# Kernel tuning notes

Measured on AMD Instinct MI355X. Metric: run time of the kernel, lower is better.

The kernel has to match this reference:

```python
import jax, jax.numpy as jnp
import numpy as np

NLAYERS = 2
K = 8          # number of attention heads
H = 64         # hidden_size (per-head QK dim)
D = 1024       # input_size; value head dim = D // K = 128
B = 4
L = 1024


def setup_inputs() -> dict:
    key = jax.random.key(0)
    ks = jax.random.split(key, 5)
    s = 1.0 / np.sqrt(D).astype(np.float32)
    return {
        "x": jax.random.normal(ks[0], (B, L, D), jnp.float32),
        "Wq": jax.random.normal(ks[1], (NLAYERS, D, H * K), jnp.float32) * s,
        "bq": jnp.zeros((NLAYERS, H * K), jnp.float32),
        "Wk": jax.random.normal(ks[2], (NLAYERS, D, H * K), jnp.float32) * s,
        "bk": jnp.zeros((NLAYERS, H * K), jnp.float32),
    }


def reference(x, Wq, bq, Wk, bk):
    Bb, Ll, Dd = x.shape
    scale = 1.0 / np.sqrt(H).astype(np.float32)
    # strictly lower-triangular causal mask: torch.tril(-1)
    causal = jnp.tril(jnp.ones((Ll, Ll), x.dtype), -1)
    neg = 1e30 * (1.0 - causal)  # additive mask
    out = x
    graphs, outputs = [], []
    for i in range(NLAYERS):
        q = jax.nn.relu(out @ Wq[i] + bq[i]).reshape(Bb, Ll, K, H)
        k = jax.nn.relu(out @ Wk[i] + bk[i]).reshape(Bb, Ll, K, H)
        att = jnp.einsum('bqkh,bskh->bkqs', q, k) * scale - neg  # [B,K,L,L]
        att = jax.nn.softmax(att, axis=-1)
        v = out.reshape(Bb, Ll, K, Dd // K)                      # value = hidden itself
        cur = jnp.einsum('bkqs,bskd->bqkd', att, v).reshape(Bb, Ll, Dd)
        out = out + cur  # residual (use_gru=False)
        graphs.append(att)
        outputs.append(out)
    return jnp.stack(graphs, 0), jnp.stack(outputs, 0)
```

## Files before the change

kernel.cpp:

```cpp
#include <hip/hip_runtime.h>
#include <cstdint>
#include <cstddef>

typedef float  f32x4  __attribute__((ext_vector_type(4)));
typedef short  bf16x8 __attribute__((ext_vector_type(8)));

constexpr int Bc = 4, Lc = 1024, Dc = 1024, Kc = 8, Hc = 64, NHc = 512;
constexpr float SCALE = 0.125f;
constexpr long long GSZ = 2LL * Bc * Kc * Lc * Lc;
constexpr long long OSZ = (long long)Bc * Lc * Dc;
constexpr int QB = 16;

__device__ __forceinline__ unsigned short f2bf(float f) {
    unsigned u = __float_as_uint(f);
    u += 0x7fffu + ((u >> 16) & 1u);
    return (unsigned short)(u >> 16);
}
__device__ __forceinline__ float bf2f(unsigned short s) {
    return __uint_as_float((unsigned)s << 16);
}

__global__ __launch_bounds__(256)
void cast_bf16(const float* __restrict__ in, unsigned short* __restrict__ outp, int n)
{
    const int i = (blockIdx.x * 256 + threadIdx.x) * 8;
    if (i >= n) return;
    float4 a = *(const float4*)(in + i);
    float4 b = *(const float4*)(in + i + 4);
    bf16x8 v;
    v[0] = (short)f2bf(a.x); v[1] = (short)f2bf(a.y);
    v[2] = (short)f2bf(a.z); v[3] = (short)f2bf(a.w);
    v[4] = (short)f2bf(b.x); v[5] = (short)f2bf(b.y);
    v[6] = (short)f2bf(b.z); v[7] = (short)f2bf(b.w);
    *(bf16x8*)(outp + i) = v;
}

__global__ __launch_bounds__(256)
void wtrans(const float* __restrict__ Wq, const float* __restrict__ Wk,
            float* __restrict__ outbase)
{
    __shared__ float Tl[64][68];
    const int z = blockIdx.z, layer = z >> 1, m = z & 1;
    const float* src = (m ? Wk : Wq) + (size_t)layer * Dc * NHc;
    unsigned short* dst = (unsigned short*)(outbase + (size_t)layer * (GSZ / 2))
                          + (size_t)m * NHc * Dc;
    const int k0 = blockIdx.x * 64, n0 = blockIdx.y * 64;
    const int t = threadIdx.x;
    {
        const int r0 = t >> 4, c0 = (t & 15) * 4;
        #pragma unroll
        for (int i = 0; i < 4; ++i)
            *(float4*)&Tl[r0 + 16 * i][c0] =
                *(const float4*)&src[(size_t)(k0 + r0 + 16 * i) * NHc + n0 + c0];
    }
    __syncthreads();
    {
        const int nn = t >> 2, ks = (t & 3) * 16;
        bf16x8 v0, v1;
        #pragma unroll
        for (int j = 0; j < 8; ++j) v0[j] = (short)f2bf(Tl[ks + j][nn]);
        #pragma unroll
        for (int j = 0; j < 8; ++j) v1[j] = (short)f2bf(Tl[ks + 8 + j][nn]);
        unsigned short* dp = dst + (size_t)(n0 + nn) * Dc + k0 + ks;
        *(bf16x8*)dp       = v0;
        *(bf16x8*)(dp + 8) = v1;
    }
}

__global__ __launch_bounds__(512)
void qk_gemm(const unsigned short* __restrict__ hidb,
             const unsigned short* __restrict__ Wtq, const unsigned short* __restrict__ Wtk,
             const float* __restrict__ bq, const float* __restrict__ bk,
             unsigned short* __restrict__ qbuf, unsigned short* __restrict__ kbuf)
{
    __shared__ unsigned short As[2][128][40];
    __shared__ unsigned short Bs[2][128][40];

    const unsigned short* Wt = blockIdx.z ? Wtk : Wtq;
    const float* bi = blockIdx.z ? bk : bq;
    unsigned short* C = blockIdx.z ? kbuf : qbuf;
    const int m0 = blockIdx.x * 128, n0 = blockIdx.y * 128;
    const int t = threadIdx.x, lane = t & 63, w = t >> 6;
    const int lr = lane & 15, lg = lane >> 4;
    const int wmloc = (w >> 2) * 64, wnloc = (w & 3) * 32;

    const int srow = t >> 2, scol = (t & 3) * 8;
    const unsigned short* Ag = hidb + (size_t)(m0 + srow) * Dc + scol;
    const unsigned short* Bg = Wt   + (size_t)(n0 + srow) * Dc + scol;

    f32x4 acc[4][2] = {};
    bf16x8 ra = *(const bf16x8*)Ag;
    bf16x8 rb = *(const bf16x8*)Bg;

    for (int it = 0; it < 32; ++it) {
        const int buf = it & 1;
        *(bf16x8*)&As[buf][srow][scol] = ra;
        *(bf16x8*)&Bs[buf][srow][scol] = rb;
        __syncthreads();
        if (it < 31) {
            ra = *(const bf16x8*)(Ag + (it + 1) * 32);
            rb = *(const bf16x8*)(Bg + (it + 1) * 32);
        }
        bf16x8 a[4], bfr[2];
        #pragma unroll
        for (int mi = 0; mi < 4; ++mi)
            a[mi] = *(const bf16x8*)&As[buf][wmloc + mi * 16 + lr][lg * 8];
        #pragma unroll
        for (int ni = 0; ni < 2; ++ni)
            bfr[ni] = *(const bf16x8*)&Bs[buf][wnloc + ni * 16 + lr][lg * 8];
        #pragma unroll
        for (int mi = 0; mi < 4; ++mi)
            #pragma unroll
            for (int ni = 0; ni < 2; ++ni)
                acc[mi][ni] = __builtin_amdgcn_mfma_f32_16x16x32_bf16(a[mi], bfr[ni], acc[mi][ni], 0, 0, 0);
    }

    #pragma unroll
    for (int ni = 0; ni < 2; ++ni) {
        const int gc = n0 + wnloc + ni * 16 + lr;
        const float bv = bi[gc];
        #pragma unroll
        for (int mi = 0; mi < 4; ++mi)
            #pragma unroll
            for (int r = 0; r < 4; ++r) {
                const int row = m0 + wmloc + mi * 16 + lg * 4 + r;
                float v = fmaxf(acc[mi][ni][r] + bv, 0.0f);
                C[(size_t)row * NHc + gc] = f2bf(v);
            }
    }
}

__global__ __launch_bounds__(512)
void attn_fused(const unsigned short* __restrict__ qbuf,
                const unsigned short* __restrict__ kbuf,
                const unsigned short* __restrict__ hidb,
                const float* __restrict__ res,
                float* __restrict__ att, float* __restrict__ outp,
                unsigned short* __restrict__ hidnext)
{
    __shared__ unsigned short Sb[QB][1040];
    __shared__ unsigned short KV[2][64][132];

    const int id = blockIdx.x;
    const int kh = id & 7, qt = (id >> 3) & 63, b = id >> 9;
    const int q0 = qt * QB;
    const int t = threadIdx.x, lane = t & 63, w = t >> 6;
    const int lr = lane & 15, lg = lane >> 4;

    bf16x8 aq[2];
    #pragma unroll
    for (int ks = 0; ks < 2; ++ks)
        aq[ks] = *(const bf16x8*)(qbuf + (size_t)(b * Lc + q0 + lr) * NHc + kh * Hc + ks * 32 + lg * 8);

    const int ccount = (q0 + QB + 63) >> 6;

    const int sh = t >> 8, srow = (t & 255) >> 2, scol = (t & 3) * 16;
    for (int cb = 0; cb < ccount; cb += 2) {
        const int cs = cb + sh;
        if (cs < ccount) {
            const unsigned short* kp = kbuf + (size_t)(b * Lc + cs * 64 + srow) * NHc + kh * Hc + scol;
            *(bf16x8*)&KV[sh][srow][scol]     = *(const bf16x8*)kp;
            *(bf16x8*)&KV[sh][srow][scol + 8] = *(const bf16x8*)(kp + 8);
        }
        __syncthreads();
        const int c = cb + (w >> 2);
        if (c < ccount) {
            const int ni = w & 3;
            f32x4 acc = {};
            #pragma unroll
            for (int ks = 0; ks < 2; ++ks) {
                bf16x8 bfr = *(const bf16x8*)&KV[w >> 2][ni * 16 + lr][ks * 32 + lg * 8];
                acc = __builtin_amdgcn_mfma_f32_16x16x32_bf16(aq[ks], bfr, acc, 0, 0, 0);
            }
            #pragma unroll
            for (int r = 0; r < 4; ++r)
                Sb[lg * 4 + r][c * 64 + ni * 16 + lr] = f2bf(acc[r] * SCALE);
        }
        __syncthreads();
    }

    #pragma unroll
    for (int i = 0; i < 2; ++i) {
        const int row = w * 2 + i, qrow = q0 + row;
        float* orow = att + ((size_t)(b * Kc + kh) * Lc + qrow) * Lc;
        if (qrow == 0) {
            const float u = 1.0f / 1024.0f;
            const short ub = (short)f2bf(u);
            bf16x8 pv8;
            #pragma unroll
            for (int j = 0; j < 8; ++j) pv8[j] = ub;
            #pragma unroll
            for (int tt = 0; tt < 2; ++tt) {
                const int col = lane * 8 + tt * 512;
                float4 o = { u, u, u, u };
                *(float4*)(orow + col) = o;
                *(float4*)(orow + col + 4) = o;
                *(bf16x8*)&Sb[row][col] = pv8;
            }
            continue;
        }
        float p[16];
        float mx = -3.0e38f;
        #pragma unroll
        for (int tt = 0; tt < 2; ++tt) {
            const int col = lane * 8 + tt * 512;
            bf16x8 v = *(const bf16x8*)&Sb[row][col];
            #pragma unroll
            for (int j = 0; j < 8; ++j) {
                const float f = bf2f((unsigned short)v[j]);
                p[tt * 8 + j] = f;
                if (col + j < qrow) mx = fmaxf(mx, f);
            }
        }
        #pragma unroll
        for (int off = 1; off < 64; off <<= 1) mx = fmaxf(mx, __shfl_xor(mx, off));
        float sum = 0.0f;
        #pragma unroll
        for (int tt = 0; tt < 2; ++tt)
            #pragma unroll
            for (int j = 0; j < 8; ++j) {
                const int col = lane * 8 + tt * 512 + j;
                const float e = (col < qrow) ? __expf(p[tt * 8 + j] - mx) : 0.0f;
                p[tt * 8 + j] = e; sum += e;
            }
        #pragma unroll
        for (int off = 1; off < 64; off <<= 1) sum += __shfl_xor(sum, off);
        const float inv = 1.0f / sum;
        #pragma unroll
        for (int tt = 0; tt < 2; ++tt) {
            const int col = lane * 8 + tt * 512;
            float4 o0 = { p[tt*8+0]*inv, p[tt*8+1]*inv, p[tt*8+2]*inv, p[tt*8+3]*inv };
            float4 o1 = { p[tt*8+4]*inv, p[tt*8+5]*inv, p[tt*8+6]*inv, p[tt*8+7]*inv };
            *(float4*)(orow + col) = o0;
            *(float4*)(orow + col + 4) = o1;
            bf16x8 pb;
            #pragma unroll
            for (int j = 0; j < 8; ++j) pb[j] = (short)f2bf(p[tt * 8 + j] * inv);
            *(bf16x8*)&Sb[row][col] = pb;
        }
    }
    __syncthreads();

    const int stiles = (qt == 0) ? 16 : ccount;
    f32x4 acc3 = {};
    const int dloc = w * 16 + lr;
    const int dcol = kh * 128 + dloc;
    const int vrow = t >> 3, vcol = (t & 7) * 16;
    for (int ti = 0; ti < stiles; ++ti) {
        const int buf = ti & 1;
        const unsigned short* vp = hidb + (size_t)(b * Lc + ti * 64 + vrow) * Dc + kh * 128 + vcol;
        *(bf16x8*)&KV[buf][vrow][vcol]     = *(const bf16x8*)vp;
        *(bf16x8*)&KV[buf][vrow][vcol + 8] = *(const bf16x8*)(vp + 8);
        __syncthreads();
        #pragma unroll
        for (int ks = 0; ks < 2; ++ks) {
            bf16x8 pa = *(const bf16x8*)&Sb[lr][ti * 64 + ks * 32 + lg * 8];
            bf16x8 bb;
            #pragma unroll
            for (int j = 0; j < 8; ++j)
                bb[j] = (short)KV[buf][ks * 32 + lg * 8 + j][dloc];
            acc3 = __builtin_amdgcn_mfma_f32_16x16x32_bf16(pa, bb, acc3, 0, 0, 0);
        }
    }

    #pragma unroll
    for (int r = 0; r < 4; ++r) {
        const size_t idx = (size_t)(b * Lc + q0 + lg * 4 + r) * Dc + dcol;
        const float v = res[idx] + acc3[r];
        outp[idx] = v;
        if (hidnext) hidnext[idx] = f2bf(v);
    }
}

extern "C" void kernel_launch(void* const* d_in, const int* in_sizes, int n_in,
                              void* d_out, int out_size, void* d_ws, size_t ws_size,
                              hipStream_t stream)
{
    const float* x  = (const float*)d_in[0];
    const float* Wq = (const float*)d_in[1];
    const float* bq = (const float*)d_in[2];
    const float* Wk = (const float*)d_in[3];
    const float* bk = (const float*)d_in[4];
    float* out = (float*)d_out;

    unsigned short* hidbA = (unsigned short*)d_ws;
    unsigned short* hidbB = hidbA + (size_t)Bc * Lc * Dc;
    unsigned short* qb    = hidbB + (size_t)Bc * Lc * Dc;
    unsigned short* kb    = qb    + (size_t)Bc * Lc * NHc;

    const int nhid = Bc * Lc * Dc;

    cast_bf16<<<nhid / 8 / 256, 256, 0, stream>>>(x, hidbA, nhid);
    wtrans<<<dim3(16, 8, 4), 256, 0, stream>>>(Wq, Wk, out);

    for (int l = 0; l < 2; ++l) {
        float* attL = out + (size_t)l * (GSZ / 2);
        float* outL = out + GSZ + (size_t)l * OSZ;
        const float* resL = l ? (out + GSZ) : x;
        const unsigned short* hidL = l ? hidbB : hidbA;
        const unsigned short* WtL = (const unsigned short*)attL;

        qk_gemm<<<dim3(32, 4, 2), 512, 0, stream>>>(
            hidL, WtL, WtL + (size_t)NHc * Dc, bq + l * NHc, bk + l * NHc, qb, kb);

        attn_fused<<<Bc * 64 * Kc, 512, 0, stream>>>(
            qb, kb, hidL, resL, attL, outL, l == 0 ? hidbB : (unsigned short*)nullptr);
    }
}
```

Before: 193.7 us.

## Use transposed bf16 hidden for PV and batch four K chunks per iteration

A new cast_tr kernel runs once per layer and writes a bf16 copy of the hidden state transposed to [B,D,L]. In the PV phase each MFMA operand then comes from one vectorized LDS read, replacing eight strided 16-bit reads. The QK score phase now stages four 64-row K chunks per barrier pair and issues two MFMAs per wave, which halves the number of barriers. In exchange, each layer pays for an extra transpose pass over the 16 MB fp32 activations.

```diff
diff --git a/kernel.cpp b/kernel.cpp
--- a/kernel.cpp
+++ b/kernel.cpp
@@ -36,6 +36,33 @@
 }
 
 __global__ __launch_bounds__(256)
+void cast_tr(const float* __restrict__ src, unsigned short* __restrict__ hidT)
+{
+    __shared__ float Tl[64][68];
+    const int b = blockIdx.z, s0 = blockIdx.x * 64, d0 = blockIdx.y * 64;
+    const int t = threadIdx.x;
+    {
+        const int r = t >> 4, c = (t & 15) * 4;
+        #pragma unroll
+        for (int i = 0; i < 4; ++i)
+            *(float4*)&Tl[r + 16 * i][c] =
+                *(const float4*)&src[((size_t)(b * Lc + s0 + r + 16 * i)) * Dc + d0 + c];
+    }
+    __syncthreads();
+    {
+        const int d = t >> 2, sc = (t & 3) * 16;
+        bf16x8 v0, v1;
+        #pragma unroll
+        for (int j = 0; j < 8; ++j) v0[j] = (short)f2bf(Tl[sc + j][d]);
+        #pragma unroll
+        for (int j = 0; j < 8; ++j) v1[j] = (short)f2bf(Tl[sc + 8 + j][d]);
+        unsigned short* dp = hidT + ((size_t)(b * Dc + d0 + d)) * Lc + s0 + sc;
+        *(bf16x8*)dp       = v0;
+        *(bf16x8*)(dp + 8) = v1;
+    }
+}
+
+__global__ __launch_bounds__(256)
 void wtrans(const float* __restrict__ Wq, const float* __restrict__ Wk,
             float* __restrict__ outbase)
 {
@@ -133,13 +160,14 @@
 __global__ __launch_bounds__(512)
 void attn_fused(const unsigned short* __restrict__ qbuf,
                 const unsigned short* __restrict__ kbuf,
-                const unsigned short* __restrict__ hidb,
+                const unsigned short* __restrict__ hidT,
                 const float* __restrict__ res,
                 float* __restrict__ att, float* __restrict__ outp,
                 unsigned short* __restrict__ hidnext)
 {
     __shared__ unsigned short Sb[QB][1040];
-    __shared__ unsigned short KV[2][64][132];
+    __shared__ unsigned short KS[4][64][66];
+    unsigned short (*VT)[128][66] = (unsigned short (*)[128][66])KS;
 
     const int id = blockIdx.x;
     const int kh = id & 7, qt = (id >> 3) & 63, b = id >> 9;
@@ -154,27 +182,35 @@
 
     const int ccount = (q0 + QB + 63) >> 6;
 
-    const int sh = t >> 8, srow = (t & 255) >> 2, scol = (t & 3) * 16;
-    for (int cb = 0; cb < ccount; cb += 2) {
-        const int cs = cb + sh;
+    const int ch = t >> 7, krow = (t & 127) >> 1, kcol = (t & 1) * 32;
+    for (int cb = 0; cb < ccount; cb += 4) {
+        const int cs = cb + ch;
         if (cs < ccount) {
-            const unsigned short* kp = kbuf + (size_t)(b * Lc + cs * 64 + srow) * NHc + kh * Hc + scol;
-            *(bf16x8*)&KV[sh][srow][scol]     = *(const bf16x8*)kp;
-            *(bf16x8*)&KV[sh][srow][scol + 8] = *(const bf16x8*)(kp + 8);
+            const unsigned short* kp = kbuf + (size_t)(b * Lc + cs * 64 + krow) * NHc + kh * Hc + kcol;
+            *(bf16x8*)&KS[ch][krow][kcol]      = *(const bf16x8*)kp;
+            *(bf16x8*)&KS[ch][krow][kcol + 8]  = *(const bf16x8*)(kp + 8);
+            *(bf16x8*)&KS[ch][krow][kcol + 16] = *(const bf16x8*)(kp + 16);
+            *(bf16x8*)&KS[ch][krow][kcol + 24] = *(const bf16x8*)(kp + 24);
         }
         __syncthreads();
-        const int c = cb + (w >> 2);
+        const int c = cb + (w >> 1);
         if (c < ccount) {
-            const int ni = w & 3;
-            f32x4 acc = {};
-            #pragma unroll
-            for (int ks = 0; ks < 2; ++ks) {
-                bf16x8 bfr = *(const bf16x8*)&KV[w >> 2][ni * 16 + lr][ks * 32 + lg * 8];
-                acc = __builtin_amdgcn_mfma_f32_16x16x32_bf16(aq[ks], bfr, acc, 0, 0, 0);
-            }
-            #pragma unroll
-            for (int r = 0; r < 4; ++r)
-                Sb[lg * 4 + r][c * 64 + ni * 16 + lr] = f2bf(acc[r] * SCALE);
+            f32x4 acc[2] = {};
+            #pragma unroll
+            for (int ks = 0; ks < 2; ++ks)
+                #pragma unroll
+                for (int i = 0; i < 2; ++i) {
+                    const int ni = (w & 1) * 2 + i;
+                    bf16x8 bfr = *(const bf16x8*)&KS[w >> 1][ni * 16 + lr][ks * 32 + lg * 8];
+                    acc[i] = __builtin_amdgcn_mfma_f32_16x16x32_bf16(aq[ks], bfr, acc[i], 0, 0, 0);
+                }
+            #pragma unroll
+            for (int i = 0; i < 2; ++i) {
+                const int ni = (w & 1) * 2 + i;
+                #pragma unroll
+                for (int r = 0; r < 4; ++r)
+                    Sb[lg * 4 + r][c * 64 + ni * 16 + lr] = f2bf(acc[i][r] * SCALE);
+            }
         }
         __syncthreads();
     }
@@ -243,22 +279,19 @@
 
     const int stiles = (qt == 0) ? 16 : ccount;
     f32x4 acc3 = {};
-    const int dloc = w * 16 + lr;
-    const int dcol = kh * 128 + dloc;
-    const int vrow = t >> 3, vcol = (t & 7) * 16;
+    const int dloc = w * 16 + lr, dcol = kh * 128 + dloc;
+    const int vd = t >> 2, vsc = (t & 3) * 16;
+    const unsigned short* vbase = hidT + (size_t)(b * Dc + kh * 128 + vd) * Lc + vsc;
     for (int ti = 0; ti < stiles; ++ti) {
         const int buf = ti & 1;
-        const unsigned short* vp = hidb + (size_t)(b * Lc + ti * 64 + vrow) * Dc + kh * 128 + vcol;
-        *(bf16x8*)&KV[buf][vrow][vcol]     = *(const bf16x8*)vp;
-        *(bf16x8*)&KV[buf][vrow][vcol + 8] = *(const bf16x8*)(vp + 8);
+        const unsigned short* vp = vbase + ti * 64;
+        *(bf16x8*)&VT[buf][vd][vsc]     = *(const bf16x8*)vp;
+        *(bf16x8*)&VT[buf][vd][vsc + 8] = *(const bf16x8*)(vp + 8);
         __syncthreads();
         #pragma unroll
         for (int ks = 0; ks < 2; ++ks) {
             bf16x8 pa = *(const bf16x8*)&Sb[lr][ti * 64 + ks * 32 + lg * 8];
-            bf16x8 bb;
-            #pragma unroll
-            for (int j = 0; j < 8; ++j)
-                bb[j] = (short)KV[buf][ks * 32 + lg * 8 + j][dloc];
+            bf16x8 bb = *(const bf16x8*)&VT[buf][dloc][ks * 32 + lg * 8];
             acc3 = __builtin_amdgcn_mfma_f32_16x16x32_bf16(pa, bb, acc3, 0, 0, 0);
         }
     }
@@ -283,27 +316,29 @@
     const float* bk = (const float*)d_in[4];
     float* out = (float*)d_out;
 
-    unsigned short* hidbA = (unsigned short*)d_ws;
-    unsigned short* hidbB = hidbA + (size_t)Bc * Lc * Dc;
-    unsigned short* qb    = hidbB + (size_t)Bc * Lc * Dc;
-    unsigned short* kb    = qb    + (size_t)Bc * Lc * NHc;
+    unsigned short* hidb = (unsigned short*)d_ws;
+    unsigned short* hidT = hidb + (size_t)Bc * Lc * Dc;
+    unsigned short* qb   = hidT + (size_t)Bc * Dc * Lc;
+    unsigned short* kb   = qb   + (size_t)Bc * Lc * NHc;
 
     const int nhid = Bc * Lc * Dc;
 
-    cast_bf16<<<nhid / 8 / 256, 256, 0, stream>>>(x, hidbA, nhid);
+    cast_bf16<<<nhid / 8 / 256, 256, 0, stream>>>(x, hidb, nhid);
     wtrans<<<dim3(16, 8, 4), 256, 0, stream>>>(Wq, Wk, out);
 
     for (int l = 0; l < 2; ++l) {
         float* attL = out + (size_t)l * (GSZ / 2);
         float* outL = out + GSZ + (size_t)l * OSZ;
         const float* resL = l ? (out + GSZ) : x;
-        const unsigned short* hidL = l ? hidbB : hidbA;
+        const float* srcL = l ? (out + GSZ) : x;
         const unsigned short* WtL = (const unsigned short*)attL;
 
+        cast_tr<<<dim3(16, 16, 4), 256, 0, stream>>>(srcL, hidT);
+
         qk_gemm<<<dim3(32, 4, 2), 512, 0, stream>>>(
-            hidL, WtL, WtL + (size_t)NHc * Dc, bq + l * NHc, bk + l * NHc, qb, kb);
+            hidb, WtL, WtL + (size_t)NHc * Dc, bq + l * NHc, bk + l * NHc, qb, kb);
 
         attn_fused<<<Bc * 64 * Kc, 512, 0, stream>>>(
-            qb, kb, hidL, resL, attL, outL, l == 0 ? hidbB : (unsigned short*)nullptr);
-    }
-}
+            qb, kb, hidT, resL, attL, outL, l == 0 ? hidb : (unsigned short*)nullptr);
+    }
+}
```

After: 304.7 us. +57.3%, slower.

## Shrink LDS via union buffer, recompute softmax exps, raise occupancy hint

Applied to the files above, without the earlier changes.

Shared memory for K and V tiles is merged into a union with tighter padding, and the score buffer padding is reduced, so more blocks can fit per CU. The launch bounds now request 6 waves-per-EU occupancy. The softmax no longer keeps a 16-float register array and instead rereads LDS and recomputes the exps, trading extra exp work for fewer registers. The QK loop now does one 128-key chunk per iteration with all 8 waves, and s_setprio wraps the MFMA sections. The V loop gains a second barrier because the tile is no longer double-buffered.

```diff
diff --git a/kernel.cpp b/kernel.cpp
--- a/kernel.cpp
+++ b/kernel.cpp
@@ -130,7 +130,7 @@
     }
 }
 
-__global__ __launch_bounds__(512)
+__global__ __launch_bounds__(512, 6)
 void attn_fused(const unsigned short* __restrict__ qbuf,
                 const unsigned short* __restrict__ kbuf,
                 const unsigned short* __restrict__ hidb,
@@ -138,8 +138,12 @@
                 float* __restrict__ att, float* __restrict__ outp,
                 unsigned short* __restrict__ hidnext)
 {
-    __shared__ unsigned short Sb[QB][1040];
-    __shared__ unsigned short KV[2][64][132];
+    __shared__ unsigned short Sb[QB][1032];
+    union KVU {
+        unsigned short KS[128][72];
+        unsigned short VS[64][136];
+    };
+    __shared__ KVU kv;
 
     const int id = blockIdx.x;
     const int kh = id & 7, qt = (id >> 3) & 63, b = id >> 9;
@@ -153,29 +157,25 @@
         aq[ks] = *(const bf16x8*)(qbuf + (size_t)(b * Lc + q0 + lr) * NHc + kh * Hc + ks * 32 + lg * 8);
 
     const int ccount = (q0 + QB + 63) >> 6;
-
-    const int sh = t >> 8, srow = (t & 255) >> 2, scol = (t & 3) * 16;
-    for (int cb = 0; cb < ccount; cb += 2) {
-        const int cs = cb + sh;
-        if (cs < ccount) {
-            const unsigned short* kp = kbuf + (size_t)(b * Lc + cs * 64 + srow) * NHc + kh * Hc + scol;
-            *(bf16x8*)&KV[sh][srow][scol]     = *(const bf16x8*)kp;
-            *(bf16x8*)&KV[sh][srow][scol + 8] = *(const bf16x8*)(kp + 8);
-        }
-        __syncthreads();
-        const int c = cb + (w >> 2);
-        if (c < ccount) {
-            const int ni = w & 3;
-            f32x4 acc = {};
-            #pragma unroll
-            for (int ks = 0; ks < 2; ++ks) {
-                bf16x8 bfr = *(const bf16x8*)&KV[w >> 2][ni * 16 + lr][ks * 32 + lg * 8];
-                acc = __builtin_amdgcn_mfma_f32_16x16x32_bf16(aq[ks], bfr, acc, 0, 0, 0);
-            }
-            #pragma unroll
-            for (int r = 0; r < 4; ++r)
-                Sb[lg * 4 + r][c * 64 + ni * 16 + lr] = f2bf(acc[r] * SCALE);
-        }
+    const int nchunk2 = (ccount + 1) >> 1;
+
+    const int krow = t >> 2, kcol = (t & 3) * 16;
+    for (int c2 = 0; c2 < nchunk2; ++c2) {
+        const unsigned short* kp = kbuf + (size_t)(b * Lc + c2 * 128 + krow) * NHc + kh * Hc + kcol;
+        *(bf16x8*)&kv.KS[krow][kcol]     = *(const bf16x8*)kp;
+        *(bf16x8*)&kv.KS[krow][kcol + 8] = *(const bf16x8*)(kp + 8);
+        __syncthreads();
+        f32x4 acc = {};
+        __builtin_amdgcn_s_setprio(1);
+        #pragma unroll
+        for (int ks = 0; ks < 2; ++ks) {
+            bf16x8 bfr = *(const bf16x8*)&kv.KS[w * 16 + lr][ks * 32 + lg * 8];
+            acc = __builtin_amdgcn_mfma_f32_16x16x32_bf16(aq[ks], bfr, acc, 0, 0, 0);
+        }
+        __builtin_amdgcn_s_setprio(0);
+        #pragma unroll
+        for (int r = 0; r < 4; ++r)
+            Sb[lg * 4 + r][c2 * 128 + w * 16 + lr] = f2bf(acc[r] * SCALE);
         __syncthreads();
     }
 
@@ -199,43 +199,44 @@
             }
             continue;
         }
-        float p[16];
         float mx = -3.0e38f;
         #pragma unroll
         for (int tt = 0; tt < 2; ++tt) {
             const int col = lane * 8 + tt * 512;
             bf16x8 v = *(const bf16x8*)&Sb[row][col];
             #pragma unroll
-            for (int j = 0; j < 8; ++j) {
-                const float f = bf2f((unsigned short)v[j]);
-                p[tt * 8 + j] = f;
-                if (col + j < qrow) mx = fmaxf(mx, f);
-            }
+            for (int j = 0; j < 8; ++j)
+                if (col + j < qrow) mx = fmaxf(mx, bf2f((unsigned short)v[j]));
         }
         #pragma unroll
         for (int off = 1; off < 64; off <<= 1) mx = fmaxf(mx, __shfl_xor(mx, off));
         float sum = 0.0f;
         #pragma unroll
-        for (int tt = 0; tt < 2; ++tt)
-            #pragma unroll
-            for (int j = 0; j < 8; ++j) {
-                const int col = lane * 8 + tt * 512 + j;
-                const float e = (col < qrow) ? __expf(p[tt * 8 + j] - mx) : 0.0f;
-                p[tt * 8 + j] = e; sum += e;
-            }
+        for (int tt = 0; tt < 2; ++tt) {
+            const int col = lane * 8 + tt * 512;
+            bf16x8 v = *(const bf16x8*)&Sb[row][col];
+            #pragma unroll
+            for (int j = 0; j < 8; ++j)
+                sum += (col + j < qrow) ? __expf(bf2f((unsigned short)v[j]) - mx) : 0.0f;
+        }
         #pragma unroll
         for (int off = 1; off < 64; off <<= 1) sum += __shfl_xor(sum, off);
         const float inv = 1.0f / sum;
         #pragma unroll
         for (int tt = 0; tt < 2; ++tt) {
             const int col = lane * 8 + tt * 512;
-            float4 o0 = { p[tt*8+0]*inv, p[tt*8+1]*inv, p[tt*8+2]*inv, p[tt*8+3]*inv };
-            float4 o1 = { p[tt*8+4]*inv, p[tt*8+5]*inv, p[tt*8+6]*inv, p[tt*8+7]*inv };
+            bf16x8 v = *(const bf16x8*)&Sb[row][col];
+            float e[8];
+            #pragma unroll
+            for (int j = 0; j < 8; ++j)
+                e[j] = (col + j < qrow) ? __expf(bf2f((unsigned short)v[j]) - mx) * inv : 0.0f;
+            float4 o0 = { e[0], e[1], e[2], e[3] };
+            float4 o1 = { e[4], e[5], e[6], e[7] };
             *(float4*)(orow + col) = o0;
             *(float4*)(orow + col + 4) = o1;
             bf16x8 pb;
             #pragma unroll
-            for (int j = 0; j < 8; ++j) pb[j] = (short)f2bf(p[tt * 8 + j] * inv);
+            for (int j = 0; j < 8; ++j) pb[j] = (short)f2bf(e[j]);
             *(bf16x8*)&Sb[row][col] = pb;
         }
     }
@@ -243,24 +244,26 @@
 
     const int stiles = (qt == 0) ? 16 : ccount;
     f32x4 acc3 = {};
-    const int dloc = w * 16 + lr;
-    const int dcol = kh * 128 + dloc;
-    const int vrow = t >> 3, vcol = (t & 7) * 16;
+    const int dloc = w * 16 + lr, dcol = kh * 128 + dloc;
+    const int vrow = t >> 3, vcol = (t & 7) * 8;
+    const unsigned short* vb = hidb + (size_t)(b * Lc + vrow) * Dc + kh * 128 + vcol;
     for (int ti = 0; ti < stiles; ++ti) {
-        const int buf = ti & 1;
-        const unsigned short* vp = hidb + (size_t)(b * Lc + ti * 64 + vrow) * Dc + kh * 128 + vcol;
-        *(bf16x8*)&KV[buf][vrow][vcol]     = *(const bf16x8*)vp;
-        *(bf16x8*)&KV[buf][vrow][vcol + 8] = *(const bf16x8*)(vp + 8);
-        __syncthreads();
+        const unsigned short* vp = vb + (size_t)ti * 64 * Dc;
+        *(bf16x8*)&kv.VS[vrow][vcol]      = *(const bf16x8*)vp;
+        *(bf16x8*)&kv.VS[vrow][vcol + 64] = *(const bf16x8*)(vp + 64);
+        __syncthreads();
+        __builtin_amdgcn_s_setprio(1);
         #pragma unroll
         for (int ks = 0; ks < 2; ++ks) {
             bf16x8 pa = *(const bf16x8*)&Sb[lr][ti * 64 + ks * 32 + lg * 8];
             bf16x8 bb;
             #pragma unroll
             for (int j = 0; j < 8; ++j)
-                bb[j] = (short)KV[buf][ks * 32 + lg * 8 + j][dloc];
+                bb[j] = (short)kv.VS[ks * 32 + lg * 8 + j][dloc];
             acc3 = __builtin_amdgcn_mfma_f32_16x16x32_bf16(pa, bb, acc3, 0, 0, 0);
         }
+        __builtin_amdgcn_s_setprio(0);
+        __syncthreads();
     }
 
     #pragma unroll
```

Result: slower. 199.1 us (+2.8%).
